# Performance work log

Measured on AMD Instinct MI355X. Metric: run time of the kernel, lower is better.

The kernel has to match this reference:

```python
import jax, jax.numpy as jnp
import numpy as np

B, S, C = 2, 2048, 512
L, H, CH = 4, 8, 64  # layers, heads, per-head channel (H*CH == C)
OD = 4 * CH          # GEGLU output_dim = channel*4 = 256
EPS = 1e-5


def layer_norm(x, g, b):
    mu = jnp.mean(x, axis=-1, keepdims=True)
    var = jnp.mean(jnp.square(x - mu), axis=-1, keepdims=True)
    return (x - mu) * jax.lax.rsqrt(var + EPS) * g + b


def gelu_tanh(g):
    # matches: 0.5 * g * (1 + tanh(g * 0.7978845608 * (1 + 0.044715 * g**2)))
    t = jnp.tanh(g * 0.7978845608 * (1.0 + 0.044715 * jnp.square(g)))
    return 0.5 * g * (1.0 + t)


def setup_inputs() -> dict:
    key = jax.random.key(0)
    ks = jax.random.split(key, 8)
    s = 0.02
    return {
        "x": jax.random.normal(ks[0], (B, S, C), jnp.float32),
        "ln_gamma": jnp.ones((L + 1, C), jnp.float32),
        "ln_beta": jnp.zeros((L + 1, C), jnp.float32),
        "Wq": jax.random.normal(ks[1], (L, C, H * CH), jnp.float32) * s,
        "Wk": jax.random.normal(ks[2], (L, C, H * CH), jnp.float32) * s,
        "Wv": jax.random.normal(ks[3], (L, C, H * CH), jnp.float32) * s,
        "Wo": jax.random.normal(ks[4], (L, H * CH, C), jnp.float32) * s,
        "bo": jnp.zeros((L, C), jnp.float32),
        "Wg": jax.random.normal(ks[5], (C, 2 * OD), jnp.float32) * s,
        "bg": jnp.zeros((2 * OD,), jnp.float32),
        "Wf": jax.random.normal(ks[6], (OD, C), jnp.float32) * s,
        "bf": jnp.zeros((C,), jnp.float32),
    }


def reference(x, ln_gamma, ln_beta, Wq, Wk, Wv, Wo, bo, Wg, bg, Wf, bf):
    scale = 1.0 / jnp.sqrt(jnp.asarray(CH, x.dtype))
    for i in range(L):
        h = layer_norm(x, ln_gamma[i], ln_beta[i])
        q = (h @ Wq[i]).reshape(B, S, H, CH)
        k = (h @ Wk[i]).reshape(B, S, H, CH)
        v = (h @ Wv[i]).reshape(B, S, H, CH)
        scores = jnp.einsum("bqhc,bkhc->bhqk", q, k) * scale
        w = jax.nn.softmax(scores, axis=-1)
        o = jnp.einsum("bhqk,bkhc->bqhc", w, v).reshape(B, S, H * CH)
        x = o @ Wo[i] + bo[i] + x
    h = layer_norm(x, ln_gamma[L], ln_beta[L])
    g = h @ Wg + bg
    a, gate = g[..., :OD], g[..., OD:]
    ff = a * gelu_tanh(gate)
    return ff @ Wf + bf + x
```

## Files before the change

kernel.cpp:

```cpp
#include <hip/hip_runtime.h>
#include <hip/hip_bf16.h>


typedef __bf16 bf16_t;
typedef __attribute__((ext_vector_type(8))) __bf16 bf16x8;
typedef __attribute__((ext_vector_type(4))) __bf16 bf16x4;
typedef __attribute__((ext_vector_type(4))) float f32x4;

#define MROWS 4096
#define KVSPLIT 2
#define NT 16

static __device__ __forceinline__ void gload_lds16(const void* g, void* l) {
  __builtin_amdgcn_global_load_lds((const __attribute__((address_space(1))) void*)g,
                                   (__attribute__((address_space(3))) void*)l, 16, 0, 0);
}
static __device__ __forceinline__ float fexp2(float x) {
  float r;
  asm("v_exp_f32 %0, %1" : "=v"(r) : "v"(x));
  return r;
}

__global__ __launch_bounds__(256) void ln_kernel(const float* __restrict__ xin,
    const float* __restrict__ gamma, const float* __restrict__ beta,
    bf16_t* __restrict__ hout)
{
  int w = threadIdx.x >> 6, l = threadIdx.x & 63;
  int row = blockIdx.x * 4 + w;
  const float* xr = xin + (size_t)row * 512 + l * 8;
  f32x4 a = *(const f32x4*)xr;
  f32x4 b2 = *(const f32x4*)(xr + 4);
  float s = a[0]+a[1]+a[2]+a[3]+b2[0]+b2[1]+b2[2]+b2[3];
  #pragma unroll
  for (int m = 1; m < 64; m <<= 1) s += __shfl_xor(s, m, 64);
  float mu = s * (1.0f/512.0f);
  float vs = 0.f;
  #pragma unroll
  for (int i = 0; i < 4; i++) { float d = a[i]-mu; vs += d*d; d = b2[i]-mu; vs += d*d; }
  #pragma unroll
  for (int m = 1; m < 64; m <<= 1) vs += __shfl_xor(vs, m, 64);
  float rstd = rsqrtf(vs * (1.0f/512.0f) + 1e-5f);
  const float* gp = gamma + l*8;
  const float* bp = beta + l*8;
  f32x4 g0 = *(const f32x4*)gp, g1 = *(const f32x4*)(gp+4);
  f32x4 p0 = *(const f32x4*)bp, p1 = *(const f32x4*)(bp+4);
  bf16x8 h;
  #pragma unroll
  for (int i = 0; i < 4; i++) {
    h[i]   = (bf16_t)((a[i]-mu)*rstd*g0[i] + p0[i]);
    h[4+i] = (bf16_t)((b2[i]-mu)*rstd*g1[i] + p1[i]);
  }
  *(bf16x8*)(hout + (size_t)row*512 + l*8) = h;
}

__global__ __launch_bounds__(256) void prep_kernel(
    const float* __restrict__ Wq, const float* __restrict__ Wk, const float* __restrict__ Wv,
    const float* __restrict__ Wo, const float* __restrict__ Wg, const float* __restrict__ Wf,
    bf16_t* __restrict__ WqkvT, bf16_t* __restrict__ WoT,
    bf16_t* __restrict__ WgT, bf16_t* __restrict__ WfT)
{
  __shared__ float tile[32][33];
  int z = blockIdx.z;
  const float* src; bf16_t* dst; int K = 512, N = 512;
  if (z < 12) {
    int lay = z & 3, which = z >> 2;
    src = (which == 0 ? Wq : which == 1 ? Wk : Wv) + (size_t)lay*512*512;
    dst = WqkvT + (size_t)lay*1536*512 + (size_t)which*512*512;
  } else if (z < 16) {
    src = Wo + (size_t)(z-12)*512*512;
    dst = WoT + (size_t)(z-12)*512*512;
  } else if (z == 16) { src = Wg; dst = WgT; }
  else { src = Wf; dst = WfT; K = 256; }
  int k0 = blockIdx.y*32, n0 = blockIdx.x*32;
  if (k0 >= K) return;
  int tx = threadIdx.x & 31, ty = threadIdx.x >> 5;
  #pragma unroll
  for (int j = 0; j < 4; j++)
    tile[ty + j*8][tx] = src[(size_t)(k0 + ty + j*8)*N + n0 + tx];
  __syncthreads();
  #pragma unroll
  for (int j = 0; j < 4; j++)
    dst[(size_t)(n0 + ty + j*8)*K + k0 + tx] = (bf16_t)tile[tx][ty + j*8];
}

template<int EPI, int BM>
__global__ __launch_bounds__(256) void gemm_bt(
    const bf16_t* __restrict__ A, const bf16_t* __restrict__ Bt,
    int N, int K,
    void* __restrict__ Cout, bf16_t* __restrict__ vTout,
    const float* __restrict__ bias, const float* __restrict__ resid, float qscale)
{
  __shared__ bf16_t As[BM*64];
  __shared__ bf16_t Bs[128*64];
  constexpr int MF = BM/32;
  int t = threadIdx.x, w = t >> 6, l = t & 63;
  int tm = blockIdx.y * BM, tn = blockIdx.x * 128;
  int wm = (w >> 1) * (BM/2), wn = (w & 1) * 64;
  f32x4 acc[MF][4] = {};
  int srow = l >> 3;
  int schunk = ((l & 7) ^ srow) * 8;
  for (int k0 = 0; k0 < K; k0 += 64) {
    __syncthreads();
    #pragma unroll
    for (int i = 0; i < BM/32; i++) {
      int rb = i*32 + w*8;
      gload_lds16(A + (size_t)(tm + rb + srow)*K + k0 + schunk, &As[rb*64]);
    }
    #pragma unroll
    for (int i = 0; i < 4; i++) {
      int rb = i*32 + w*8;
      gload_lds16(Bt + (size_t)(tn + rb + srow)*K + k0 + schunk, &Bs[rb*64]);
    }
    __syncthreads();
    #pragma unroll
    for (int kk = 0; kk < 2; kk++) {
      bf16x8 af[MF], bfr[4];
      #pragma unroll
      for (int mf = 0; mf < MF; mf++) {
        int row = wm + mf*16 + (l & 15);
        int off = (kk*32 + (l >> 4)*8) ^ ((row & 7) << 3);
        af[mf] = *(const bf16x8*)&As[row*64 + off];
      }
      #pragma unroll
      for (int nf = 0; nf < 4; nf++) {
        int row = wn + nf*16 + (l & 15);
        int off = (kk*32 + (l >> 4)*8) ^ ((row & 7) << 3);
        bfr[nf] = *(const bf16x8*)&Bs[row*64 + off];
      }
      #pragma unroll
      for (int mf = 0; mf < MF; mf++)
        #pragma unroll
        for (int nf = 0; nf < 4; nf++)
          acc[mf][nf] = __builtin_amdgcn_mfma_f32_16x16x32_bf16(af[mf], bfr[nf], acc[mf][nf], 0, 0, 0);
    }
  }
  int colb = tn + wn + (l & 15);
  int rowb = tm + wm + ((l >> 4) << 2);
  if (EPI == 0 && tn >= 1024) {
    #pragma unroll
    for (int mf = 0; mf < MF; mf++)
      #pragma unroll
      for (int nf = 0; nf < 4; nf++) {
        int col = colb + nf*16;
        int hh = (col - 1024) >> 6, ch = (col - 1024) & 63;
        int row = rowb + mf*16;
        int bb = row >> 11, sdx = row & 2047;
        bf16x4 pk;
        #pragma unroll
        for (int r = 0; r < 4; r++) pk[r] = (bf16_t)acc[mf][nf][r];
        *(bf16x4*)&vTout[(((size_t)bb*8 + hh)*64 + ch)*2048 + sdx] = pk;
      }
    return;
  }
  #pragma unroll
  for (int mf = 0; mf < MF; mf++)
    #pragma unroll
    for (int nf = 0; nf < 4; nf++)
      #pragma unroll
      for (int r = 0; r < 4; r++) {
        int row = rowb + mf*16 + r;
        int col = colb + nf*16;
        float v = acc[mf][nf][r];
        if (EPI == 0) {
          if (col < 512) v *= qscale;
          ((bf16_t*)Cout)[(size_t)row*1024 + col] = (bf16_t)v;
        } else if (EPI == 1) {
          ((float*)Cout)[(size_t)row*N + col] = v + bias[col] + resid[(size_t)row*N + col];
        } else {
          ((float*)Cout)[(size_t)row*N + col] = v + bias[col];
        }
      }
}

__global__ __launch_bounds__(256) void attn_kernel(const bf16_t* __restrict__ qkv,
                                                   const bf16_t* __restrict__ vT,
                                                   float* __restrict__ Ows,
                                                   float* __restrict__ lws)
{
  __shared__ bf16_t Ks[64*64];
  __shared__ bf16_t Vs[64*64];
  __shared__ bf16_t Ps[4*16*72];
  int t = threadIdx.x, w = t >> 6, l = t & 63;
  int q0 = blockIdx.x * 64, h = blockIdx.y;
  int b = blockIdx.z >> 1, sp = blockIdx.z & 1;
  size_t rbase = (size_t)b * 2048;
  int kvb = sp * (2048/KVSPLIT);
  int lq = l & 15, hi = l >> 4;
  int srow = l >> 3;
  int schunk = ((l & 7) ^ srow) * 8;
  int rb0 = w*16, rb1 = w*16 + 8;
  const bf16_t* kb  = qkv + rbase*1024 + 512 + h*64;
  const bf16_t* vtb = vT + ((size_t)(b*8 + h)*64)*2048 + kvb;
  const bf16_t* qp = qkv + (rbase + q0 + w*16 + lq)*1024 + h*64 + hi*8;
  bf16x8 aq0 = *(const bf16x8*)qp;
  bf16x8 aq1 = *(const bf16x8*)(qp + 32);
  gload_lds16(kb + (size_t)(kvb + rb0 + srow)*1024 + schunk, &Ks[rb0*64]);
  gload_lds16(kb + (size_t)(kvb + rb1 + srow)*1024 + schunk, &Ks[rb1*64]);
  gload_lds16(vtb + (size_t)(rb0 + srow)*2048 + schunk, &Vs[rb0*64]);
  gload_lds16(vtb + (size_t)(rb1 + srow)*2048 + schunk, &Vs[rb1*64]);
  asm volatile("s_waitcnt vmcnt(0)" ::: "memory");
  __builtin_amdgcn_s_barrier();

  int pw = w * 16 * 72;
  f32x4 accO[4] = {};
  f32x4 lacc = {};
  bf16x8 ones;
  #pragma unroll
  for (int e = 0; e < 8; e++) ones[e] = (bf16_t)1.0f;
  int swz = (lq & 7) << 3;

  for (int tt = 0; tt < NT; ++tt) {
    f32x4 s4[4] = {};
    bf16x8 vv[8];
    #pragma unroll
    for (int kk = 0; kk < 2; kk++) {
      int off = (kk*32 + hi*8) ^ swz;
      bf16x8 aq = kk ? aq1 : aq0;
      #pragma unroll
      for (int nf = 0; nf < 4; nf++) {
        bf16x8 bk = *(const bf16x8*)&Ks[(nf*16 + lq)*64 + off];
        s4[nf] = __builtin_amdgcn_mfma_f32_16x16x32_bf16(aq, bk, s4[nf], 0, 0, 0);
        vv[kk*4+nf] = *(const bf16x8*)&Vs[(nf*16 + lq)*64 + off];
      }
    }
    asm volatile("s_waitcnt lgkmcnt(0)" ::: "memory");
    __builtin_amdgcn_s_barrier();
    __builtin_amdgcn_sched_barrier(0);
    if (tt < NT-1) {
      int kv1 = kvb + (tt + 1) * 64;
      gload_lds16(kb + (size_t)(kv1 + rb0 + srow)*1024 + schunk, &Ks[rb0*64]);
      gload_lds16(kb + (size_t)(kv1 + rb1 + srow)*1024 + schunk, &Ks[rb1*64]);
      gload_lds16(vtb + (size_t)(rb0 + srow)*2048 + (tt+1)*64 + schunk, &Vs[rb0*64]);
      gload_lds16(vtb + (size_t)(rb1 + srow)*2048 + (tt+1)*64 + schunk, &Vs[rb1*64]);
    }
    #pragma unroll
    for (int nf = 0; nf < 4; nf++)
      #pragma unroll
      for (int r = 0; r < 4; r++)
        Ps[pw + (hi*4 + r)*72 + nf*16 + lq] = (bf16_t)fexp2(s4[nf][r]);
    #pragma unroll
    for (int kk = 0; kk < 2; kk++) {
      bf16x8 pa = *(const bf16x8*)&Ps[pw + lq*72 + kk*32 + hi*8];
      lacc = __builtin_amdgcn_mfma_f32_16x16x32_bf16(pa, ones, lacc, 0, 0, 0);
      #pragma unroll
      for (int nf = 0; nf < 4; nf++)
        accO[nf] = __builtin_amdgcn_mfma_f32_16x16x32_bf16(pa, vv[kk*4+nf], accO[nf], 0, 0, 0);
    }
    if (tt < NT-1) {
      asm volatile("s_waitcnt vmcnt(0)" ::: "memory");
      __builtin_amdgcn_s_barrier();
    }
  }
  float* op = Ows + (size_t)sp*MROWS*512 + (rbase + q0 + w*16 + hi*4)*512 + h*64 + lq;
  #pragma unroll
  for (int nf = 0; nf < 4; nf++)
    #pragma unroll
    for (int r = 0; r < 4; r++)
      op[(size_t)r*512 + nf*16] = accO[nf][r];
  if (lq == 0) {
    size_t rowb = rbase + q0 + w*16 + hi*4;
    #pragma unroll
    for (int r = 0; r < 4; r++)
      lws[(size_t)sp*MROWS*8 + (rowb + r)*8 + h] = lacc[r];
  }
}

__global__ __launch_bounds__(256) void combine_kernel(const float* __restrict__ Ows,
                                                      const float* __restrict__ lws,
                                                      bf16_t* __restrict__ obuf)
{
  int idx = blockIdx.x * 256 + threadIdx.x;
  int row = idx >> 7, c4 = (idx & 127) * 4;
  f32x4 o0 = *(const f32x4*)&Ows[(size_t)row*512 + c4];
  f32x4 o1 = *(const f32x4*)&Ows[(size_t)(MROWS + row)*512 + c4];
  int h = c4 >> 6;
  float li = 1.0f / (lws[row*8 + h] + lws[MROWS*8 + row*8 + h]);
  bf16x4 o;
  #pragma unroll
  for (int i = 0; i < 4; i++) o[i] = (bf16_t)((o0[i] + o1[i]) * li);
  *(bf16x4*)&obuf[(size_t)row*512 + c4] = o;
}

__global__ __launch_bounds__(256) void gelu_kernel(const float* __restrict__ g,
                                                   bf16_t* __restrict__ ff)
{
  int idx = blockIdx.x * 256 + threadIdx.x;
  int row = idx >> 6;
  int c = (idx & 63) * 4;
  const float* gr = g + (size_t)row*512;
  f32x4 a = *(const f32x4*)(gr + c);
  f32x4 u = *(const f32x4*)(gr + 256 + c);
  bf16x4 o4;
  #pragma unroll
  for (int i = 0; i < 4; i++) {
    float x = u[i];
    float tt = tanhf(0.7978845608f * x * (1.0f + 0.044715f * x * x));
    o4[i] = (bf16_t)(a[i] * 0.5f * x * (1.0f + tt));
  }
  *(bf16x4*)(ff + (size_t)row*256 + c) = o4;
}

extern "C" void kernel_launch(void* const* d_in, const int* in_sizes, int n_in,
                              void* d_out, int out_size, void* d_ws, size_t ws_size,
                              hipStream_t stream)
{
  const float* x     = (const float*)d_in[0];
  const float* gamma = (const float*)d_in[1];
  const float* beta  = (const float*)d_in[2];
  const float* Wq    = (const float*)d_in[3];
  const float* Wk    = (const float*)d_in[4];
  const float* Wv    = (const float*)d_in[5];
  const float* Wo    = (const float*)d_in[6];
  const float* bo    = (const float*)d_in[7];
  const float* Wg    = (const float*)d_in[8];
  const float* bg    = (const float*)d_in[9];
  const float* Wf    = (const float*)d_in[10];
  const float* bf    = (const float*)d_in[11];

  char* ws = (char*)d_ws;
  float*  xcur  = (float*)ws;
  bf16_t* hbuf  = (bf16_t*)(ws + (8u<<20));
  bf16_t* qkv   = (bf16_t*)(ws + (12u<<20));
  bf16_t* vT    = (bf16_t*)(ws + (20u<<20));
  bf16_t* obuf  = (bf16_t*)(ws + (24u<<20));
  bf16_t* WqkvT = (bf16_t*)(ws + (28u<<20));
  bf16_t* WoT   = (bf16_t*)(ws + (34u<<20));
  bf16_t* WgT   = (bf16_t*)(ws + (36u<<20));
  bf16_t* WfT   = (bf16_t*)(ws + (36u<<20) + (512u<<10));
  float*  lws   = (float*)(ws + (37u<<20));
  float*  Ows   = (float*)(ws + (40u<<20));
  float*  gbuf  = (float*)qkv;
  bf16_t* ffb   = obuf;

  const float QSCALE = 0.125f * 1.44269504f;

  prep_kernel<<<dim3(16,16,18), 256, 0, stream>>>(Wq,Wk,Wv,Wo,Wg,Wf,WqkvT,WoT,WgT,WfT);
  hipMemcpyAsync(xcur, x, (size_t)MROWS*512*4, hipMemcpyDeviceToDevice, stream);

  for (int lay = 0; lay < 4; lay++) {
    ln_kernel<<<1024, 256, 0, stream>>>(xcur, gamma + lay*512, beta + lay*512, hbuf);
    gemm_bt<0,64><<<dim3(12,64), 256, 0, stream>>>(hbuf, WqkvT + (size_t)lay*1536*512,
                                                   1536, 512, qkv, vT, nullptr, nullptr, QSCALE);
    attn_kernel<<<dim3(32,8,2*KVSPLIT), 256, 0, stream>>>(qkv, vT, Ows, lws);
    combine_kernel<<<2048, 256, 0, stream>>>(Ows, lws, obuf);
    gemm_bt<1,64><<<dim3(4,64), 256, 0, stream>>>(obuf, WoT + (size_t)lay*512*512,
                                                  512, 512, xcur, nullptr, bo + lay*512, xcur, 1.0f);
  }
  ln_kernel<<<1024, 256, 0, stream>>>(xcur, gamma + 4*512, beta + 4*512, hbuf);
  gemm_bt<2,64><<<dim3(4,64), 256, 0, stream>>>(hbuf, WgT, 512, 512, gbuf, nullptr, bg, nullptr, 1.0f);
  gelu_kernel<<<1024, 256, 0, stream>>>(gbuf, ffb);
  gemm_bt<1,64><<<dim3(4,64), 256, 0, stream>>>(ffb, WfT, 512, 256, d_out, nullptr, bf, xcur, 1.0f);
}
```

Measured before the change: 413.2 us.

## Remap block IDs for XCD-aware locality and store attention partials in bf16

GEMM and attention launches now use 1D grids. The block index is remapped so that consecutive logical tiles land on the same XCD (blockIdx mod 8 picks the chiplet), which should improve L2 reuse of shared K/V and weight tiles. Separately, the split-KV partial outputs are written and read as bf16 instead of fp32, halving the traffic between the attention and combine kernels. The cost is some extra rounding in the unnormalized partial sums, and the remap assumes the grid size is a multiple of 8.

New measurement: 389.4 us. -5.8%, faster.

```diff
diff --git a/kernel.cpp b/kernel.cpp
--- a/kernel.cpp
+++ b/kernel.cpp
@@ -83,7 +83,7 @@
     dst[(size_t)(n0 + ty + j*8)*K + k0 + tx] = (bf16_t)tile[tx][ty + j*8];
 }
 
-template<int EPI, int BM>
+template<int EPI, int BM, int NX>
 __global__ __launch_bounds__(256) void gemm_bt(
     const bf16_t* __restrict__ A, const bf16_t* __restrict__ Bt,
     int N, int K,
@@ -93,8 +93,11 @@
   __shared__ bf16_t As[BM*64];
   __shared__ bf16_t Bs[128*64];
   constexpr int MF = BM/32;
+  int cpx = gridDim.x >> 3;
+  int logical = (blockIdx.x & 7) * cpx + (blockIdx.x >> 3);
+  int bx = logical % NX, by = logical / NX;
   int t = threadIdx.x, w = t >> 6, l = t & 63;
-  int tm = blockIdx.y * BM, tn = blockIdx.x * 128;
+  int tm = by * BM, tn = bx * 128;
   int wm = (w >> 1) * (BM/2), wn = (w & 1) * 64;
   f32x4 acc[MF][4] = {};
   int srow = l >> 3;
@@ -174,15 +177,19 @@
 
 __global__ __launch_bounds__(256) void attn_kernel(const bf16_t* __restrict__ qkv,
                                                    const bf16_t* __restrict__ vT,
-                                                   float* __restrict__ Ows,
+                                                   bf16_t* __restrict__ Ows,
                                                    float* __restrict__ lws)
 {
   __shared__ bf16_t Ks[64*64];
   __shared__ bf16_t Vs[64*64];
   __shared__ bf16_t Ps[4*16*72];
   int t = threadIdx.x, w = t >> 6, l = t & 63;
-  int q0 = blockIdx.x * 64, h = blockIdx.y;
-  int b = blockIdx.z >> 1, sp = blockIdx.z & 1;
+  int logical = (blockIdx.x & 7) * 128 + (blockIdx.x >> 3);
+  int q0 = (logical & 31) * 64;
+  int group = logical >> 5;
+  int h = group & 7;
+  int bz = group >> 3;
+  int b = bz >> 1, sp = bz & 1;
   size_t rbase = (size_t)b * 2048;
   int kvb = sp * (2048/KVSPLIT);
   int lq = l & 15, hi = l >> 4;
@@ -251,12 +258,12 @@
       __builtin_amdgcn_s_barrier();
     }
   }
-  float* op = Ows + (size_t)sp*MROWS*512 + (rbase + q0 + w*16 + hi*4)*512 + h*64 + lq;
+  bf16_t* op = Ows + (size_t)sp*MROWS*512 + (rbase + q0 + w*16 + hi*4)*512 + h*64 + lq;
   #pragma unroll
   for (int nf = 0; nf < 4; nf++)
     #pragma unroll
     for (int r = 0; r < 4; r++)
-      op[(size_t)r*512 + nf*16] = accO[nf][r];
+      op[(size_t)r*512 + nf*16] = (bf16_t)accO[nf][r];
   if (lq == 0) {
     size_t rowb = rbase + q0 + w*16 + hi*4;
     #pragma unroll
@@ -265,19 +272,19 @@
   }
 }
 
-__global__ __launch_bounds__(256) void combine_kernel(const float* __restrict__ Ows,
+__global__ __launch_bounds__(256) void combine_kernel(const bf16_t* __restrict__ Ows,
                                                       const float* __restrict__ lws,
                                                       bf16_t* __restrict__ obuf)
 {
   int idx = blockIdx.x * 256 + threadIdx.x;
   int row = idx >> 7, c4 = (idx & 127) * 4;
-  f32x4 o0 = *(const f32x4*)&Ows[(size_t)row*512 + c4];
-  f32x4 o1 = *(const f32x4*)&Ows[(size_t)(MROWS + row)*512 + c4];
+  bf16x4 o0 = *(const bf16x4*)&Ows[(size_t)row*512 + c4];
+  bf16x4 o1 = *(const bf16x4*)&Ows[(size_t)(MROWS + row)*512 + c4];
   int h = c4 >> 6;
   float li = 1.0f / (lws[row*8 + h] + lws[MROWS*8 + row*8 + h]);
   bf16x4 o;
   #pragma unroll
-  for (int i = 0; i < 4; i++) o[i] = (bf16_t)((o0[i] + o1[i]) * li);
+  for (int i = 0; i < 4; i++) o[i] = (bf16_t)(((float)o0[i] + (float)o1[i]) * li);
   *(bf16x4*)&obuf[(size_t)row*512 + c4] = o;
 }
 
@@ -328,7 +335,7 @@
   bf16_t* WgT   = (bf16_t*)(ws + (36u<<20));
   bf16_t* WfT   = (bf16_t*)(ws + (36u<<20) + (512u<<10));
   float*  lws   = (float*)(ws + (37u<<20));
-  float*  Ows   = (float*)(ws + (40u<<20));
+  bf16_t* Ows   = (bf16_t*)(ws + (40u<<20));
   float*  gbuf  = (float*)qkv;
   bf16_t* ffb   = obuf;
 
@@ -339,15 +346,15 @@
 
   for (int lay = 0; lay < 4; lay++) {
     ln_kernel<<<1024, 256, 0, stream>>>(xcur, gamma + lay*512, beta + lay*512, hbuf);
-    gemm_bt<0,64><<<dim3(12,64), 256, 0, stream>>>(hbuf, WqkvT + (size_t)lay*1536*512,
-                                                   1536, 512, qkv, vT, nullptr, nullptr, QSCALE);
-    attn_kernel<<<dim3(32,8,2*KVSPLIT), 256, 0, stream>>>(qkv, vT, Ows, lws);
+    gemm_bt<0,64,12><<<768, 256, 0, stream>>>(hbuf, WqkvT + (size_t)lay*1536*512,
+                                              1536, 512, qkv, vT, nullptr, nullptr, QSCALE);
+    attn_kernel<<<1024, 256, 0, stream>>>(qkv, vT, Ows, lws);
     combine_kernel<<<2048, 256, 0, stream>>>(Ows, lws, obuf);
-    gemm_bt<1,64><<<dim3(4,64), 256, 0, stream>>>(obuf, WoT + (size_t)lay*512*512,
-                                                  512, 512, xcur, nullptr, bo + lay*512, xcur, 1.0f);
+    gemm_bt<1,64,4><<<256, 256, 0, stream>>>(obuf, WoT + (size_t)lay*512*512,
+                                             512, 512, xcur, nullptr, bo + lay*512, xcur, 1.0f);
   }
   ln_kernel<<<1024, 256, 0, stream>>>(xcur, gamma + 4*512, beta + 4*512, hbuf);
-  gemm_bt<2,64><<<dim3(4,64), 256, 0, stream>>>(hbuf, WgT, 512, 512, gbuf, nullptr, bg, nullptr, 1.0f);
+  gemm_bt<2,64,4><<<256, 256, 0, stream>>>(hbuf, WgT, 512, 512, gbuf, nullptr, bg, nullptr, 1.0f);
   gelu_kernel<<<1024, 256, 0, stream>>>(gbuf, ffb);
-  gemm_bt<1,64><<<dim3(4,64), 256, 0, stream>>>(ffb, WfT, 512, 256, d_out, nullptr, bf, xcur, 1.0f);
-}
+  gemm_bt<1,64,4><<<256, 256, 0, stream>>>(ffb, WfT, 512, 256, d_out, nullptr, bf, xcur, 1.0f);
+}
```
